# Performance work log

Hardware: AMD Instinct MI355X
Metric: run time of the kernel (lower is better)

Reference implementation:

```python
import jax, jax.numpy as jnp
import numpy as np

LN_EPS = 1e-5
DEG_EPS = 1e-12


def setup_inputs() -> dict:
    key = jax.random.key(0)
    k1, k2, k3, k4 = jax.random.split(key, 4)
    N, E, D = 100000, 1000000, 64
    x = jax.random.normal(k1, (N, D), dtype=jnp.float32)
    edge_index = jax.random.randint(k2, (2, E), 0, N, dtype=jnp.int64)
    edge_weight = jax.random.uniform(k3, (E,), dtype=jnp.float32)
    # xavier_uniform for Linear(D, D): bound = sqrt(6/(D+D))
    bound = float(np.sqrt(6.0 / (D + D)))
    W = jax.random.uniform(k4, (D, D), dtype=jnp.float32, minval=-bound, maxval=bound)
    b = jnp.zeros((D,), dtype=jnp.float32)
    ln_gamma = jnp.ones((D,), dtype=jnp.float32)
    ln_beta = jnp.zeros((D,), dtype=jnp.float32)
    return {"x": x, "edge_index": edge_index, "edge_weight": edge_weight,
            "W": W, "b": b, "ln_gamma": ln_gamma, "ln_beta": ln_beta}


def reference(x, edge_index, edge_weight, W, b, ln_gamma, ln_beta):
    N = x.shape[0]
    # --- add self loops with weight 1.0 ---
    diag = jnp.arange(N, dtype=edge_index.dtype)
    ei = jnp.concatenate([edge_index, jnp.stack([diag, diag], axis=0)], axis=1)
    ew = jnp.concatenate([edge_weight.astype(jnp.float32),
                          jnp.ones((N,), dtype=jnp.float32)], axis=0)
    row, col = ei[0], ei[1]
    # --- renormalized adjacency weights: D^{-1/2}(A+I)D^{-1/2} ---
    deg = jax.ops.segment_sum(ew, row, num_segments=N)  # [N]
    deg_inv_sqrt = (deg + DEG_EPS) ** -0.5
    nw = ew * deg_inv_sqrt[row] * deg_inv_sqrt[col]     # [E+N]
    # --- SpMM: gather, scale, segment-sum ---
    msg = x[col] * nw[:, None].astype(x.dtype)          # [E+N, D]
    h = jax.ops.segment_sum(msg, row, num_segments=N)   # [N, D]
    # --- linear + gelu (exact erf) + layernorm + residual ---
    y = h @ W.T + b
    y = jax.nn.gelu(y, approximate=False)
    mean = jnp.mean(y, axis=-1, keepdims=True)
    var = jnp.mean(jnp.square(y - mean), axis=-1, keepdims=True)
    y = (y - mean) * jax.lax.rsqrt(var + LN_EPS) * ln_gamma + ln_beta
    return y + x
```

## Files before the change

kernel.cpp:

```cpp
#include <hip/hip_runtime.h>
#include <math.h>

#define DEG_EPS 1e-12f
#define LN_EPS  1e-5f
#define BROWS   128
#define CAPA    1536
#define MAXBKT  1024
#define CHUNK   2048
#define SCAP    896

typedef __attribute__((ext_vector_type(8))) short bf16x8;
typedef __attribute__((ext_vector_type(4))) float f32x4;

__device__ __forceinline__ short f2bf(float f) {
    unsigned u = __float_as_uint(f);
    u += 0x7FFF + ((u >> 16) & 1);
    return (short)(u >> 16);
}
__device__ __forceinline__ float bf_lo(unsigned u) { return __uint_as_float(u << 16); }
__device__ __forceinline__ float bf_hi(unsigned u) { return __uint_as_float(u & 0xFFFF0000u); }


__global__ __launch_bounds__(512) void k_bin(
    const int* __restrict__ rows, const int* __restrict__ cols,
    const float* __restrict__ ew,
    int* __restrict__ bktcnt, int2* __restrict__ bktbuf,
    int E, int NBKT)
{
    __shared__ int hist[MAXBKT];
    __shared__ int base_s[MAXBKT];
    __shared__ int cur[MAXBKT];
    __shared__ int srow[CHUNK];
    const int t = threadIdx.x;
    const int e0 = blockIdx.x * CHUNK;
    const int tc = min(E - e0, CHUNK);

    for (int i = t; i < NBKT; i += 512) { hist[i] = 0; cur[i] = 0; }
    __syncthreads();
    for (int i = t; i < tc; i += 512) {
        int r = rows[e0 + i];
        srow[i] = r;
        atomicAdd(&hist[r >> 7], 1);
    }
    __syncthreads();
    for (int i = t; i < NBKT; i += 512) {
        int h = hist[i];
        base_s[i] = h ? atomicAdd(&bktcnt[i], h) : 0;
    }
    __syncthreads();
    for (int i = t; i < tc; i += 512) {
        int r = srow[i];
        int bkt = r >> 7;
        int slot = base_s[bkt] + atomicAdd(&cur[bkt], 1);
        if (slot < CAPA)
            bktbuf[(size_t)bkt * CAPA + slot] =
                make_int2(((r & 127) << 17) | cols[e0 + i],
                          __float_as_int(ew[e0 + i]));
    }
}

__global__ __launch_bounds__(256) void k_xw_dis(
    const int* __restrict__ bktcnt, const int2* __restrict__ bktbuf,
    const float* __restrict__ x, const float* __restrict__ W,
    unsigned short* __restrict__ xwb, float* __restrict__ dis, int N)
{
    __shared__ unsigned sfx[BROWS];
    const int t = threadIdx.x;
    const int bkt = blockIdx.x;
    const int r0 = bkt * BROWS;
    if (t < BROWS) sfx[t] = 0;
    __syncthreads();

    int nb = bktcnt[bkt];
    if (nb > CAPA) nb = CAPA;
    const int2* buf = bktbuf + (size_t)bkt * CAPA;
    for (int i = t; i < nb; i += 256) {
        int2 e = buf[i];
        atomicAdd(&sfx[(e.x >> 17) & 127],
                  __float2uint_rn(__int_as_float(e.y) * 16777216.0f));
    }

    const int lane = t & 63, wv = t >> 6;
    const int m = lane & 15, q = lane >> 4;
    bf16x8 bfrag[4][2];
#pragma unroll
    for (int f = 0; f < 4; ++f)
#pragma unroll
        for (int s = 0; s < 2; ++s) {
            const float4* wp = (const float4*)(W + (f * 16 + m) * 64 + s * 32 + q * 8);
            float4 lo = wp[0], hi = wp[1];
            bf16x8 v;
            v[0] = f2bf(lo.x); v[1] = f2bf(lo.y); v[2] = f2bf(lo.z); v[3] = f2bf(lo.w);
            v[4] = f2bf(hi.x); v[5] = f2bf(hi.y); v[6] = f2bf(hi.z); v[7] = f2bf(hi.w);
            bfrag[f][s] = v;
        }
#pragma unroll
    for (int tl = 0; tl < 2; ++tl) {
        int n0 = r0 + (wv * 2 + tl) * 16;
        if (n0 < N) {
            int nr = n0 + m; if (nr >= N) nr = N - 1;
            bf16x8 afrag[2];
#pragma unroll
            for (int s = 0; s < 2; ++s) {
                const float4* xp = (const float4*)(x + (size_t)nr * 64 + s * 32 + q * 8);
                float4 lo = xp[0], hi = xp[1];
                bf16x8 v;
                v[0] = f2bf(lo.x); v[1] = f2bf(lo.y); v[2] = f2bf(lo.z); v[3] = f2bf(lo.w);
                v[4] = f2bf(hi.x); v[5] = f2bf(hi.y); v[6] = f2bf(hi.z); v[7] = f2bf(hi.w);
                afrag[s] = v;
            }
#pragma unroll
            for (int f = 0; f < 4; ++f) {
                f32x4 acc = {0.f, 0.f, 0.f, 0.f};
                acc = __builtin_amdgcn_mfma_f32_16x16x32_bf16(afrag[0], bfrag[f][0], acc, 0, 0, 0);
                acc = __builtin_amdgcn_mfma_f32_16x16x32_bf16(afrag[1], bfrag[f][1], acc, 0, 0, 0);
#pragma unroll
                for (int r4 = 0; r4 < 4; ++r4) {
                    int node = n0 + q * 4 + r4;
                    if (node < N)
                        xwb[(size_t)node * 64 + f * 16 + m] = (unsigned short)f2bf(acc[r4]);
                }
            }
        }
    }

    __syncthreads();
    if (t < BROWS && r0 + t < N) {
        float deg = 1.0f + (float)sfx[t] * (1.0f / 16777216.0f);
        dis[r0 + t] = rsqrtf(deg + DEG_EPS);
    }
}

__global__ __launch_bounds__(256) void k_spmm_fused(
    const int* __restrict__ bktcnt, const int2* __restrict__ bktbuf,
    const float* __restrict__ dis, const uint2* __restrict__ xw4,
    const float* __restrict__ x, const float* __restrict__ bias,
    const float* __restrict__ gamma, const float* __restrict__ beta,
    float* __restrict__ out, int N)
{
    __shared__ int2  srt[SCAP];
    __shared__ int   cnt[64], off[64], cur[64], sc[64];
    __shared__ float sdis[64];
    const int t = threadIdx.x;
    const int bkt  = blockIdx.x >> 1;
    const int half = blockIdx.x & 1;
    const int r0 = bkt * BROWS + half * 64;

    if (t < 64) {
        cnt[t] = 0; cur[t] = 0;
        int r = r0 + t;
        sdis[t] = (r < N) ? dis[r] : 1.0f;
    }
    __syncthreads();

    int nb = bktcnt[bkt];
    if (nb > CAPA) nb = CAPA;
    const int2* buf = bktbuf + (size_t)bkt * CAPA;

    int2 eb[6];
#pragma unroll
    for (int u = 0; u < 6; ++u) {
        int i = t + u * 256;
        eb[u] = (i < nb) ? buf[i] : make_int2(-1, 0);
    }
#pragma unroll
    for (int u = 0; u < 6; ++u)
        if (eb[u].x >= 0) {
            int rq = (eb[u].x >> 17) & 127;
            if ((rq >> 6) != half) eb[u].x = -1;
            else atomicAdd(&cnt[rq & 63], 1);
        }
    __syncthreads();

    int v = 0;
    if (t < 64) { v = cnt[t]; sc[t] = v; }
    __syncthreads();
    for (int o = 1; o < 64; o <<= 1) {
        int u2 = 0;
        if (t < 64 && t >= o) u2 = sc[t - o];
        __syncthreads();
        if (t < 64) sc[t] += u2;
        __syncthreads();
    }
    if (t < 64) off[t] = sc[t] - v;
    __syncthreads();

#pragma unroll
    for (int u = 0; u < 6; ++u)
        if (eb[u].x >= 0) {
            int rl = (eb[u].x >> 17) & 63;
            int c  = eb[u].x & 0x1FFFF;
            float w = __int_as_float(eb[u].y) * sdis[rl] * dis[c];
            int pos = off[rl] + atomicAdd(&cur[rl], 1);
            if (pos < SCAP)
                srt[pos] = make_int2(c, __float_as_int(w));
        }
    __syncthreads();

    const int lane = t & 63, wv = t >> 6;
    const int k  = lane & 15;
    const int qh = lane >> 4;

    for (int i = 0; i < 16; ++i) {
        const int rl = wv * 16 + i;
        const int row = r0 + rl;
        if (row >= N) break;

        int rcnt = cnt[rl]; if (rcnt > 64) rcnt = 64;
        int rbase = off[rl];
        float s = sdis[rl];

        float a0 = 0.f, a1 = 0.f, a2 = 0.f, a3 = 0.f;
        if (qh == 0) {
            float s2 = s * s;
            uint2 vv = xw4[(size_t)row * 16 + k];
            a0 = bf_lo(vv.x) * s2; a1 = bf_hi(vv.x) * s2;
            a2 = bf_lo(vv.y) * s2; a3 = bf_hi(vv.y) * s2;
        }

        int c = 0; float w = 0.f;
        if (lane < rcnt) {
            int2 m = srt[rbase + lane];
            c = m.x;
            w = __int_as_float(m.y);
        }

        int tmax = (rcnt + 3) >> 2;
        int tt = 0;
        for (; tt + 2 <= tmax; tt += 2) {
            int j0 = 4 * tt + qh, j1 = j0 + 4;
            int   c0 = __shfl(c, j0, 64);
            float w0 = __shfl(w, j0, 64);
            int   c1 = __shfl(c, j1, 64);
            float w1 = __shfl(w, j1, 64);
            uint2 v0 = xw4[(size_t)c0 * 16 + k];
            uint2 v1 = xw4[(size_t)c1 * 16 + k];
            a0 = fmaf(bf_lo(v0.x), w0, a0); a1 = fmaf(bf_hi(v0.x), w0, a1);
            a2 = fmaf(bf_lo(v0.y), w0, a2); a3 = fmaf(bf_hi(v0.y), w0, a3);
            a0 = fmaf(bf_lo(v1.x), w1, a0); a1 = fmaf(bf_hi(v1.x), w1, a1);
            a2 = fmaf(bf_lo(v1.y), w1, a2); a3 = fmaf(bf_hi(v1.y), w1, a3);
        }
        if (tt < tmax) {
            int j = 4 * tt + qh;
            int   cc = __shfl(c, j, 64);
            float ww = __shfl(w, j, 64);
            uint2 vv = xw4[(size_t)cc * 16 + k];
            a0 = fmaf(bf_lo(vv.x), ww, a0); a1 = fmaf(bf_hi(vv.x), ww, a1);
            a2 = fmaf(bf_lo(vv.y), ww, a2); a3 = fmaf(bf_hi(vv.y), ww, a3);
        }

#pragma unroll
        for (int mk = 16; mk < 64; mk <<= 1) {
            a0 += __shfl_xor(a0, mk, 64);
            a1 += __shfl_xor(a1, mk, 64);
            a2 += __shfl_xor(a2, mk, 64);
            a3 += __shfl_xor(a3, mk, 64);
        }

        float a = (qh == 0) ? a0 : (qh == 1) ? a1 : (qh == 2) ? a2 : a3;
        int f = 4 * k + qh;
        a += bias[f];
        a = 0.5f * a * (1.0f + erff(a * 0.70710678118654752f));

        float sum = a, ssq = a * a;
#pragma unroll
        for (int mk = 1; mk < 64; mk <<= 1) {
            sum += __shfl_xor(sum, mk, 64);
            ssq += __shfl_xor(ssq, mk, 64);
        }
        float mean = sum * (1.0f / 64.0f);
        float var  = fmaxf(ssq * (1.0f / 64.0f) - mean * mean, 0.0f);
        float rs   = rsqrtf(var + LN_EPS);
        float nrm  = (a - mean) * rs;

        float nv = __shfl(nrm, ((lane & 3) << 4) | (lane >> 2), 64);
        out[(size_t)row * 64 + lane] =
            nv * gamma[lane] + beta[lane] + x[(size_t)row * 64 + lane];
    }
}

extern "C" void kernel_launch(void* const* d_in, const int* in_sizes, int n_in,
                              void* d_out, int out_size, void* d_ws, size_t ws_size,
                              hipStream_t stream) {
    const float* x   = (const float*)d_in[0];
    const int*   ei  = (const int*)  d_in[1];
    const float* ew  = (const float*)d_in[2];
    const float* W   = (const float*)d_in[3];
    const float* b   = (const float*)d_in[4];
    const float* g   = (const float*)d_in[5];
    const float* bt  = (const float*)d_in[6];
    float* out = (float*)d_out;

    const int N = in_sizes[0] / 64;
    const int E = in_sizes[1] / 2;
    const int* rows = ei;
    const int* cols = ei + E;
    const int NBKT = (N + BROWS - 1) / BROWS;

    char* w8 = (char*)d_ws;
    int2*  bktbuf = (int2*)w8;                    w8 += (size_t)NBKT * CAPA * 8;
    unsigned short* xwb = (unsigned short*)w8;    w8 += (size_t)N * 128;
    float* dis    = (float*)w8;                   w8 += (size_t)N * 4;
    int*   bktcnt = (int*)w8;

    hipMemsetAsync(bktcnt, 0, (size_t)NBKT * 4, stream);

    const int binB = (E + CHUNK - 1) / CHUNK;
    k_bin<<<binB, 512, 0, stream>>>(rows, cols, ew, bktcnt, bktbuf, E, NBKT);

    k_xw_dis<<<NBKT, 256, 0, stream>>>(bktcnt, bktbuf, x, W, xwb, dis, N);

    const int spmmB = (N + 63) / 64;
    k_spmm_fused<<<spmmB, 256, 0, stream>>>(
        bktcnt, bktbuf, dis, (const uint2*)xwb, x, b, g, bt, out, N);
}
```

Before: 175.2 us.

## Fuse all stages into one cooperative persistent kernel with grid syncs

Replaces the memset plus three kernel launches with a single cooperative kernel that zeroes the counters, then runs edge binning on a subset of blocks while the remaining blocks compute the bf16 XW product concurrently. Grid-wide syncs separate the degree/normalisation phase and the fused SpMM+GELU+LayerNorm phase, with shared memory unioned across phases. This removes launch gaps and overlaps binning with the matmul, at the cost of grid.sync overhead, a persistent grid limited by occupancy, and a bin phase running on fewer blocks with 256 threads instead of 512.

```diff
diff --git a/kernel.cpp b/kernel.cpp
--- a/kernel.cpp
+++ b/kernel.cpp
@@ -1,13 +1,16 @@
 #include <hip/hip_runtime.h>
+#include <hip/hip_cooperative_groups.h>
 #include <math.h>
 
 #define DEG_EPS 1e-12f
 #define LN_EPS  1e-5f
 #define BROWS   128
 #define CAPA    1536
-#define MAXBKT  1024
+#define NBKTC   800
 #define CHUNK   2048
 #define SCAP    896
+
+namespace cg = cooperative_groups;
 
 typedef __attribute__((ext_vector_type(8))) short bf16x8;
 typedef __attribute__((ext_vector_type(4))) float f32x4;
@@ -21,83 +24,78 @@
 __device__ __forceinline__ float bf_hi(unsigned u) { return __uint_as_float(u & 0xFFFF0000u); }
 
 
-__global__ __launch_bounds__(512) void k_bin(
+struct BinS { int hist[NBKTC]; int base[NBKTC]; int cur[NBKTC]; int srow[CHUNK]; };
+struct DisS { unsigned sfx[BROWS]; };
+struct SpS  { int2 srt[SCAP]; int cnt[64]; int off[64]; int cur[64]; int sc[64]; float sdis[64]; };
+union  SMem { BinS b; DisS d; SpS s; };
+
+__global__ __launch_bounds__(256, 7) void k_mega(
     const int* __restrict__ rows, const int* __restrict__ cols,
-    const float* __restrict__ ew,
+    const float* __restrict__ ew, const float* __restrict__ x,
+    const float* __restrict__ W, const float* __restrict__ bias,
+    const float* __restrict__ gamma, const float* __restrict__ beta,
+    float* __restrict__ out,
     int* __restrict__ bktcnt, int2* __restrict__ bktbuf,
-    int E, int NBKT)
+    unsigned short* __restrict__ xwb, float* __restrict__ dis,
+    int E, int N, int NBKT, int Ntiles, int nChunks, int binB, int nHB)
 {
-    __shared__ int hist[MAXBKT];
-    __shared__ int base_s[MAXBKT];
-    __shared__ int cur[MAXBKT];
-    __shared__ int srow[CHUNK];
+    __shared__ SMem sm;
     const int t = threadIdx.x;
-    const int e0 = blockIdx.x * CHUNK;
-    const int tc = min(E - e0, CHUNK);
-
-    for (int i = t; i < NBKT; i += 512) { hist[i] = 0; cur[i] = 0; }
-    __syncthreads();
-    for (int i = t; i < tc; i += 512) {
-        int r = rows[e0 + i];
-        srow[i] = r;
-        atomicAdd(&hist[r >> 7], 1);
-    }
-    __syncthreads();
-    for (int i = t; i < NBKT; i += 512) {
-        int h = hist[i];
-        base_s[i] = h ? atomicAdd(&bktcnt[i], h) : 0;
-    }
-    __syncthreads();
-    for (int i = t; i < tc; i += 512) {
-        int r = srow[i];
-        int bkt = r >> 7;
-        int slot = base_s[bkt] + atomicAdd(&cur[bkt], 1);
-        if (slot < CAPA)
-            bktbuf[(size_t)bkt * CAPA + slot] =
-                make_int2(((r & 127) << 17) | cols[e0 + i],
-                          __float_as_int(ew[e0 + i]));
-    }
-}
-
-__global__ __launch_bounds__(256) void k_xw_dis(
-    const int* __restrict__ bktcnt, const int2* __restrict__ bktbuf,
-    const float* __restrict__ x, const float* __restrict__ W,
-    unsigned short* __restrict__ xwb, float* __restrict__ dis, int N)
-{
-    __shared__ unsigned sfx[BROWS];
-    const int t = threadIdx.x;
-    const int bkt = blockIdx.x;
-    const int r0 = bkt * BROWS;
-    if (t < BROWS) sfx[t] = 0;
-    __syncthreads();
-
-    int nb = bktcnt[bkt];
-    if (nb > CAPA) nb = CAPA;
-    const int2* buf = bktbuf + (size_t)bkt * CAPA;
-    for (int i = t; i < nb; i += 256) {
-        int2 e = buf[i];
-        atomicAdd(&sfx[(e.x >> 17) & 127],
-                  __float2uint_rn(__int_as_float(e.y) * 16777216.0f));
-    }
-
-    const int lane = t & 63, wv = t >> 6;
-    const int m = lane & 15, q = lane >> 4;
-    bf16x8 bfrag[4][2];
-#pragma unroll
-    for (int f = 0; f < 4; ++f)
-#pragma unroll
-        for (int s = 0; s < 2; ++s) {
-            const float4* wp = (const float4*)(W + (f * 16 + m) * 64 + s * 32 + q * 8);
-            float4 lo = wp[0], hi = wp[1];
-            bf16x8 v;
-            v[0] = f2bf(lo.x); v[1] = f2bf(lo.y); v[2] = f2bf(lo.z); v[3] = f2bf(lo.w);
-            v[4] = f2bf(hi.x); v[5] = f2bf(hi.y); v[6] = f2bf(hi.z); v[7] = f2bf(hi.w);
-            bfrag[f][s] = v;
-        }
-#pragma unroll
-    for (int tl = 0; tl < 2; ++tl) {
-        int n0 = r0 + (wv * 2 + tl) * 16;
-        if (n0 < N) {
+    const int lane = t & 63;
+    cg::grid_group grid = cg::this_grid();
+
+    for (int i = blockIdx.x * 256 + t; i < NBKT; i += gridDim.x * 256)
+        bktcnt[i] = 0;
+    grid.sync();
+
+    if ((int)blockIdx.x < binB) {
+        for (int chunk = blockIdx.x; chunk < nChunks; chunk += binB) {
+            const int e0 = chunk * CHUNK;
+            const int tc = min(E - e0, CHUNK);
+            for (int i = t; i < NBKT; i += 256) { sm.b.hist[i] = 0; sm.b.cur[i] = 0; }
+            __syncthreads();
+            for (int i = t; i < tc; i += 256) {
+                int r = rows[e0 + i];
+                sm.b.srow[i] = r;
+                atomicAdd(&sm.b.hist[r >> 7], 1);
+            }
+            __syncthreads();
+            for (int i = t; i < NBKT; i += 256) {
+                int h = sm.b.hist[i];
+                sm.b.base[i] = h ? atomicAdd(&bktcnt[i], h) : 0;
+            }
+            __syncthreads();
+            for (int i = t; i < tc; i += 256) {
+                int r = sm.b.srow[i];
+                int bkt = r >> 7;
+                int slot = sm.b.base[bkt] + atomicAdd(&sm.b.cur[bkt], 1);
+                if (slot < CAPA)
+                    bktbuf[(size_t)bkt * CAPA + slot] =
+                        make_int2(((r & 127) << 17) | cols[e0 + i],
+                                  __float_as_int(ew[e0 + i]));
+            }
+            __syncthreads();
+        }
+    } else {
+        const int m = lane & 15;
+        const int q = lane >> 4;
+        const int nwv = (gridDim.x - binB) * 4;
+        const int wave = (blockIdx.x - binB) * 4 + (t >> 6);
+
+        bf16x8 bfrag[4][2];
+#pragma unroll
+        for (int f = 0; f < 4; ++f)
+#pragma unroll
+            for (int s = 0; s < 2; ++s) {
+                const float4* wp = (const float4*)(W + (f * 16 + m) * 64 + s * 32 + q * 8);
+                float4 lo = wp[0], hi = wp[1];
+                bf16x8 v;
+                v[0] = f2bf(lo.x); v[1] = f2bf(lo.y); v[2] = f2bf(lo.z); v[3] = f2bf(lo.w);
+                v[4] = f2bf(hi.x); v[5] = f2bf(hi.y); v[6] = f2bf(hi.z); v[7] = f2bf(hi.w);
+                bfrag[f][s] = v;
+            }
+        for (int tl = wave; tl < Ntiles; tl += nwv) {
+            int n0 = tl * 16;
             int nr = n0 + m; if (nr >= N) nr = N - 1;
             bf16x8 afrag[2];
 #pragma unroll
@@ -123,159 +121,166 @@
             }
         }
     }
-
-    __syncthreads();
-    if (t < BROWS && r0 + t < N) {
-        float deg = 1.0f + (float)sfx[t] * (1.0f / 16777216.0f);
-        dis[r0 + t] = rsqrtf(deg + DEG_EPS);
+    grid.sync();
+
+    for (int bkt = blockIdx.x; bkt < NBKT; bkt += gridDim.x) {
+        if (t < BROWS) sm.d.sfx[t] = 0;
+        __syncthreads();
+        int nb = bktcnt[bkt];
+        if (nb > CAPA) nb = CAPA;
+        const int2* buf = bktbuf + (size_t)bkt * CAPA;
+        for (int i = t; i < nb; i += 256) {
+            int2 e = buf[i];
+            atomicAdd(&sm.d.sfx[(e.x >> 17) & 127],
+                      __float2uint_rn(__int_as_float(e.y) * 16777216.0f));
+        }
+        __syncthreads();
+        int r = bkt * BROWS + t;
+        if (t < BROWS && r < N) {
+            float deg = 1.0f + (float)sm.d.sfx[t] * (1.0f / 16777216.0f);
+            dis[r] = rsqrtf(deg + DEG_EPS);
+        }
+        __syncthreads();
     }
-}
-
-__global__ __launch_bounds__(256) void k_spmm_fused(
-    const int* __restrict__ bktcnt, const int2* __restrict__ bktbuf,
-    const float* __restrict__ dis, const uint2* __restrict__ xw4,
-    const float* __restrict__ x, const float* __restrict__ bias,
-    const float* __restrict__ gamma, const float* __restrict__ beta,
-    float* __restrict__ out, int N)
-{
-    __shared__ int2  srt[SCAP];
-    __shared__ int   cnt[64], off[64], cur[64], sc[64];
-    __shared__ float sdis[64];
-    const int t = threadIdx.x;
-    const int bkt  = blockIdx.x >> 1;
-    const int half = blockIdx.x & 1;
-    const int r0 = bkt * BROWS + half * 64;
-
-    if (t < 64) {
-        cnt[t] = 0; cur[t] = 0;
-        int r = r0 + t;
-        sdis[t] = (r < N) ? dis[r] : 1.0f;
-    }
-    __syncthreads();
-
-    int nb = bktcnt[bkt];
-    if (nb > CAPA) nb = CAPA;
-    const int2* buf = bktbuf + (size_t)bkt * CAPA;
-
-    int2 eb[6];
-#pragma unroll
-    for (int u = 0; u < 6; ++u) {
-        int i = t + u * 256;
-        eb[u] = (i < nb) ? buf[i] : make_int2(-1, 0);
-    }
-#pragma unroll
-    for (int u = 0; u < 6; ++u)
-        if (eb[u].x >= 0) {
-            int rq = (eb[u].x >> 17) & 127;
-            if ((rq >> 6) != half) eb[u].x = -1;
-            else atomicAdd(&cnt[rq & 63], 1);
-        }
-    __syncthreads();
-
-    int v = 0;
-    if (t < 64) { v = cnt[t]; sc[t] = v; }
-    __syncthreads();
-    for (int o = 1; o < 64; o <<= 1) {
-        int u2 = 0;
-        if (t < 64 && t >= o) u2 = sc[t - o];
-        __syncthreads();
-        if (t < 64) sc[t] += u2;
-        __syncthreads();
-    }
-    if (t < 64) off[t] = sc[t] - v;
-    __syncthreads();
-
-#pragma unroll
-    for (int u = 0; u < 6; ++u)
-        if (eb[u].x >= 0) {
-            int rl = (eb[u].x >> 17) & 63;
-            int c  = eb[u].x & 0x1FFFF;
-            float w = __int_as_float(eb[u].y) * sdis[rl] * dis[c];
-            int pos = off[rl] + atomicAdd(&cur[rl], 1);
-            if (pos < SCAP)
-                srt[pos] = make_int2(c, __float_as_int(w));
-        }
-    __syncthreads();
-
-    const int lane = t & 63, wv = t >> 6;
-    const int k  = lane & 15;
-    const int qh = lane >> 4;
-
-    for (int i = 0; i < 16; ++i) {
-        const int rl = wv * 16 + i;
-        const int row = r0 + rl;
-        if (row >= N) break;
-
-        int rcnt = cnt[rl]; if (rcnt > 64) rcnt = 64;
-        int rbase = off[rl];
-        float s = sdis[rl];
-
-        float a0 = 0.f, a1 = 0.f, a2 = 0.f, a3 = 0.f;
-        if (qh == 0) {
-            float s2 = s * s;
-            uint2 vv = xw4[(size_t)row * 16 + k];
-            a0 = bf_lo(vv.x) * s2; a1 = bf_hi(vv.x) * s2;
-            a2 = bf_lo(vv.y) * s2; a3 = bf_hi(vv.y) * s2;
-        }
-
-        int c = 0; float w = 0.f;
-        if (lane < rcnt) {
-            int2 m = srt[rbase + lane];
-            c = m.x;
-            w = __int_as_float(m.y);
-        }
-
-        int tmax = (rcnt + 3) >> 2;
-        int tt = 0;
-        for (; tt + 2 <= tmax; tt += 2) {
-            int j0 = 4 * tt + qh, j1 = j0 + 4;
-            int   c0 = __shfl(c, j0, 64);
-            float w0 = __shfl(w, j0, 64);
-            int   c1 = __shfl(c, j1, 64);
-            float w1 = __shfl(w, j1, 64);
-            uint2 v0 = xw4[(size_t)c0 * 16 + k];
-            uint2 v1 = xw4[(size_t)c1 * 16 + k];
-            a0 = fmaf(bf_lo(v0.x), w0, a0); a1 = fmaf(bf_hi(v0.x), w0, a1);
-            a2 = fmaf(bf_lo(v0.y), w0, a2); a3 = fmaf(bf_hi(v0.y), w0, a3);
-            a0 = fmaf(bf_lo(v1.x), w1, a0); a1 = fmaf(bf_hi(v1.x), w1, a1);
-            a2 = fmaf(bf_lo(v1.y), w1, a2); a3 = fmaf(bf_hi(v1.y), w1, a3);
-        }
-        if (tt < tmax) {
-            int j = 4 * tt + qh;
-            int   cc = __shfl(c, j, 64);
-            float ww = __shfl(w, j, 64);
-            uint2 vv = xw4[(size_t)cc * 16 + k];
-            a0 = fmaf(bf_lo(vv.x), ww, a0); a1 = fmaf(bf_hi(vv.x), ww, a1);
-            a2 = fmaf(bf_lo(vv.y), ww, a2); a3 = fmaf(bf_hi(vv.y), ww, a3);
-        }
-
-#pragma unroll
-        for (int mk = 16; mk < 64; mk <<= 1) {
-            a0 += __shfl_xor(a0, mk, 64);
-            a1 += __shfl_xor(a1, mk, 64);
-            a2 += __shfl_xor(a2, mk, 64);
-            a3 += __shfl_xor(a3, mk, 64);
-        }
-
-        float a = (qh == 0) ? a0 : (qh == 1) ? a1 : (qh == 2) ? a2 : a3;
-        int f = 4 * k + qh;
-        a += bias[f];
-        a = 0.5f * a * (1.0f + erff(a * 0.70710678118654752f));
-
-        float sum = a, ssq = a * a;
-#pragma unroll
-        for (int mk = 1; mk < 64; mk <<= 1) {
-            sum += __shfl_xor(sum, mk, 64);
-            ssq += __shfl_xor(ssq, mk, 64);
-        }
-        float mean = sum * (1.0f / 64.0f);
-        float var  = fmaxf(ssq * (1.0f / 64.0f) - mean * mean, 0.0f);
-        float rs   = rsqrtf(var + LN_EPS);
-        float nrm  = (a - mean) * rs;
-
-        float nv = __shfl(nrm, ((lane & 3) << 4) | (lane >> 2), 64);
-        out[(size_t)row * 64 + lane] =
-            nv * gamma[lane] + beta[lane] + x[(size_t)row * 64 + lane];
+    grid.sync();
+
+    for (int hb = blockIdx.x; hb < nHB; hb += gridDim.x) {
+        const int bkt  = hb >> 1;
+        const int half = hb & 1;
+        const int r0 = bkt * BROWS + half * 64;
+
+        if (t < 64) {
+            sm.s.cnt[t] = 0; sm.s.cur[t] = 0;
+            int r = r0 + t;
+            sm.s.sdis[t] = (r < N) ? dis[r] : 1.0f;
+        }
+        __syncthreads();
+
+        int nb = bktcnt[bkt];
+        if (nb > CAPA) nb = CAPA;
+        const int2* buf = bktbuf + (size_t)bkt * CAPA;
+
+        int2 eb[6];
+#pragma unroll
+        for (int u = 0; u < 6; ++u) {
+            int i = t + u * 256;
+            eb[u] = (i < nb) ? buf[i] : make_int2(-1, 0);
+        }
+#pragma unroll
+        for (int u = 0; u < 6; ++u)
+            if (eb[u].x >= 0) {
+                int rq = (eb[u].x >> 17) & 127;
+                if ((rq >> 6) != half) eb[u].x = -1;
+                else atomicAdd(&sm.s.cnt[rq & 63], 1);
+            }
+        __syncthreads();
+
+        int v = 0;
+        if (t < 64) { v = sm.s.cnt[t]; sm.s.sc[t] = v; }
+        __syncthreads();
+        for (int o = 1; o < 64; o <<= 1) {
+            int u2 = 0;
+            if (t < 64 && t >= o) u2 = sm.s.sc[t - o];
+            __syncthreads();
+            if (t < 64) sm.s.sc[t] += u2;
+            __syncthreads();
+        }
+        if (t < 64) sm.s.off[t] = sm.s.sc[t] - v;
+        __syncthreads();
+
+#pragma unroll
+        for (int u = 0; u < 6; ++u)
+            if (eb[u].x >= 0) {
+                int rl = (eb[u].x >> 17) & 63;
+                int c  = eb[u].x & 0x1FFFF;
+                float w = __int_as_float(eb[u].y) * sm.s.sdis[rl] * dis[c];
+                int pos = sm.s.off[rl] + atomicAdd(&sm.s.cur[rl], 1);
+                if (pos < SCAP)
+                    sm.s.srt[pos] = make_int2(c, __float_as_int(w));
+            }
+        __syncthreads();
+
+        const int wv = t >> 6;
+        const int k  = lane & 15;
+        const int qh = lane >> 4;
+
+        for (int i = 0; i < 16; ++i) {
+            const int rl = wv * 16 + i;
+            const int row = r0 + rl;
+            if (row >= N) break;
+
+            int rcnt = sm.s.cnt[rl]; if (rcnt > 64) rcnt = 64;
+            int rbase = sm.s.off[rl];
+            float s = sm.s.sdis[rl];
+
+            float a0 = 0.f, a1 = 0.f, a2 = 0.f, a3 = 0.f;
+            if (qh == 0) {
+                float s2 = s * s;
+                uint2 vv = ((const uint2*)xwb)[(size_t)row * 16 + k];
+                a0 = bf_lo(vv.x) * s2; a1 = bf_hi(vv.x) * s2;
+                a2 = bf_lo(vv.y) * s2; a3 = bf_hi(vv.y) * s2;
+            }
+
+            int c = 0; float w = 0.f;
+            if (lane < rcnt) {
+                int2 m = sm.s.srt[rbase + lane];
+                c = m.x;
+                w = __int_as_float(m.y);
+            }
+
+            int tmax = (rcnt + 3) >> 2;
+            int tt = 0;
+            for (; tt + 2 <= tmax; tt += 2) {
+                int j0 = 4 * tt + qh, j1 = j0 + 4;
+                int   c0 = __shfl(c, j0, 64);
+                float w0 = __shfl(w, j0, 64);
+                int   c1 = __shfl(c, j1, 64);
+                float w1 = __shfl(w, j1, 64);
+                uint2 v0 = ((const uint2*)xwb)[(size_t)c0 * 16 + k];
+                uint2 v1 = ((const uint2*)xwb)[(size_t)c1 * 16 + k];
+                a0 = fmaf(bf_lo(v0.x), w0, a0); a1 = fmaf(bf_hi(v0.x), w0, a1);
+                a2 = fmaf(bf_lo(v0.y), w0, a2); a3 = fmaf(bf_hi(v0.y), w0, a3);
+                a0 = fmaf(bf_lo(v1.x), w1, a0); a1 = fmaf(bf_hi(v1.x), w1, a1);
+                a2 = fmaf(bf_lo(v1.y), w1, a2); a3 = fmaf(bf_hi(v1.y), w1, a3);
+            }
+            if (tt < tmax) {
+                int j = 4 * tt + qh;
+                int   cc = __shfl(c, j, 64);
+                float ww = __shfl(w, j, 64);
+                uint2 vv = ((const uint2*)xwb)[(size_t)cc * 16 + k];
+                a0 = fmaf(bf_lo(vv.x), ww, a0); a1 = fmaf(bf_hi(vv.x), ww, a1);
+                a2 = fmaf(bf_lo(vv.y), ww, a2); a3 = fmaf(bf_hi(vv.y), ww, a3);
+            }
+
+#pragma unroll
+            for (int mk = 16; mk < 64; mk <<= 1) {
+                a0 += __shfl_xor(a0, mk, 64);
+                a1 += __shfl_xor(a1, mk, 64);
+                a2 += __shfl_xor(a2, mk, 64);
+                a3 += __shfl_xor(a3, mk, 64);
+            }
+
+            float a = (qh == 0) ? a0 : (qh == 1) ? a1 : (qh == 2) ? a2 : a3;
+            int f = 4 * k + qh;
+            a += bias[f];
+            a = 0.5f * a * (1.0f + erff(a * 0.70710678118654752f));
+
+            float sum = a, ssq = a * a;
+#pragma unroll
+            for (int mk = 1; mk < 64; mk <<= 1) {
+                sum += __shfl_xor(sum, mk, 64);
+                ssq += __shfl_xor(ssq, mk, 64);
+            }
+            float mean = sum * (1.0f / 64.0f);
+            float var  = fmaxf(ssq * (1.0f / 64.0f) - mean * mean, 0.0f);
+            float rs   = rsqrtf(var + LN_EPS);
+            float nrm  = (a - mean) * rs;
+
+            float nv = __shfl(nrm, ((lane & 3) << 4) | (lane >> 2), 64);
+            out[(size_t)row * 64 + lane] =
+                nv * gamma[lane] + beta[lane] + x[(size_t)row * 64 + lane];
+        }
+        __syncthreads();
     }
 }
 
@@ -295,7 +300,10 @@
     const int E = in_sizes[1] / 2;
     const int* rows = ei;
     const int* cols = ei + E;
-    const int NBKT = (N + BROWS - 1) / BROWS;
+    int Ntiles  = (N + 15) / 16;
+    int NBKT    = (N + BROWS - 1) / BROWS;
+    int nChunks = (E + CHUNK - 1) / CHUNK;
+    int nHB     = (N + 63) / 64;
 
     char* w8 = (char*)d_ws;
     int2*  bktbuf = (int2*)w8;                    w8 += (size_t)NBKT * CAPA * 8;
@@ -303,14 +311,30 @@
     float* dis    = (float*)w8;                   w8 += (size_t)N * 4;
     int*   bktcnt = (int*)w8;
 
-    hipMemsetAsync(bktcnt, 0, (size_t)NBKT * 4, stream);
-
-    const int binB = (E + CHUNK - 1) / CHUNK;
-    k_bin<<<binB, 512, 0, stream>>>(rows, cols, ew, bktcnt, bktbuf, E, NBKT);
-
-    k_xw_dis<<<NBKT, 256, 0, stream>>>(bktcnt, bktbuf, x, W, xwb, dis, N);
-
-    const int spmmB = (N + 63) / 64;
-    k_spmm_fused<<<spmmB, 256, 0, stream>>>(
-        bktcnt, bktbuf, dis, (const uint2*)xwb, x, b, g, bt, out, N);
+    static int gGrid = 0;
+    if (gGrid == 0) {
+        int maxb = 0;
+        if (hipOccupancyMaxActiveBlocksPerMultiprocessor(&maxb, k_mega, 256, 0)
+                != hipSuccess || maxb < 1)
+            maxb = 4;
+        hipDeviceProp_t prop;
+        int cu = 256;
+        if (hipGetDeviceProperties(&prop, 0) == hipSuccess && prop.multiProcessorCount > 0)
+            cu = prop.multiProcessorCount;
+        long gr = (long)maxb * cu;
+        if (gr < 256) gr = 256;
+        gGrid = (int)gr;
+    }
+    int grid = gGrid < nHB ? gGrid : nHB;
+    int binB = nChunks < grid / 3 ? nChunks : grid / 3;
+
+    void* kargs[] = {
+        (void*)&rows, (void*)&cols, (void*)&ew, (void*)&x, (void*)&W,
+        (void*)&b, (void*)&g, (void*)&bt, (void*)&out,
+        (void*)&bktcnt, (void*)&bktbuf, (void*)&xwb, (void*)&dis,
+        (void*)&E, (void*)&N, (void*)&NBKT, (void*)&Ntiles,
+        (void*)&nChunks, (void*)&binB, (void*)&nHB
+    };
+    hipLaunchCooperativeKernel((const void*)k_mega, dim3(grid), dim3(256),
+                               kargs, 0, stream);
 }
```

After: 452.0 us. +158.0%, slower.
